# Performance work log

Measured on AMD Instinct MI355X. Metric: run time of the kernel, lower is better.

Reference implementation:

```python
import jax, jax.numpy as jnp
import numpy as np

N, IN_DIM, N_HEADS, HID, OUT = 4096, 512, 8, 64, 128


def setup_inputs() -> dict:
    key = jax.random.key(0)
    k0, k1, k2, k3 = jax.random.split(key, 4)
    x = jax.random.normal(k0, (N, IN_DIM), dtype=jnp.float32)
    adj = jax.random.randint(k1, (N, N), 0, 2).astype(jnp.int32)
    Wh = jax.random.normal(k2, (N_HEADS, IN_DIM, HID), dtype=jnp.float32) * 0.02
    bh = jnp.zeros((N_HEADS, HID), dtype=jnp.float32)
    Wo = jax.random.normal(k3, (N_HEADS * HID, OUT), dtype=jnp.float32) * 0.02
    bo = jnp.zeros((OUT,), dtype=jnp.float32)
    return {"x": x, "adj": adj, "Wh": Wh, "bh": bh, "Wo": Wo, "bo": bo}


def _masked_attn(q, k, v, mask):
    # adjacency-masked scaled dot-product attention; q,k,v: [..., n, d]
    d = q.shape[-1]
    scores = jnp.einsum('...nd,...md->...nm', q, k) / jnp.sqrt(jnp.asarray(d, q.dtype))
    scores = jnp.where(mask, scores, jnp.asarray(-1e9, q.dtype))
    attn = jax.nn.softmax(scores, axis=-1)
    return jnp.einsum('...nm,...md->...nd', attn, v)


def reference(x, adj, Wh, bh, Wo, bo):
    mask = adj > 0  # [N, N]
    # per-head: Linear -> masked attention -> ELU (dropout is identity in eval)
    h = jnp.einsum('ni,hid->hnd', x, Wh) + bh[:, None, :]        # [H, N, D]
    heads = jax.nn.elu(_masked_attn(h, h, h, mask[None]))        # [H, N, D]
    cat = jnp.transpose(heads, (1, 0, 2)).reshape(x.shape[0], -1)  # [N, H*D]
    z = cat @ Wo + bo                                            # [N, OUT]
    out = jax.nn.elu(_masked_attn(z, z, z, mask))                # [N, OUT]
    return jax.nn.log_softmax(out, axis=1)
```

## Files before the change

### kernel.cpp

```cpp
#include <hip/hip_runtime.h>
#include <stdint.h>


#define NN 4096
#define IND 512
#define NH 8
#define HD 64
#define OD 128
#define S1 2
#define KSPLIT 8

typedef __bf16 bf16;
typedef bf16 bf16x8 __attribute__((ext_vector_type(8)));
typedef float f32x4 __attribute__((ext_vector_type(4)));
typedef unsigned short u16;
typedef unsigned long long u64;

__device__ __forceinline__ u16 f2bf(float f) {
  union { float f; unsigned u; } v; v.f = f;
  return (u16)((v.u + 0x7fffu + ((v.u >> 16) & 1u)) >> 16);
}

__device__ __forceinline__ f32x4 mfma16(bf16x8 a, bf16x8 b, f32x4 c) {
  return __builtin_amdgcn_mfma_f32_16x16x32_bf16(a, b, c, 0, 0, 0);
}

__global__ void k_h(const float* __restrict__ x, const float* __restrict__ Wh,
                    const float* __restrict__ bh, u16* __restrict__ h,
                    u16* __restrict__ hT) {
  const int head = blockIdx.y;
  const int d = threadIdx.x & 63;
  const int wv = threadIdx.x >> 6;
  const int n0 = blockIdx.x * 32 + wv * 8;
  const float* __restrict__ W = Wh + head * IND * HD;
  const float b0 = bh[head * HD + d];
  float acc[8];
  #pragma unroll
  for (int r = 0; r < 8; ++r) acc[r] = b0;
  #pragma unroll 2
  for (int i = 0; i < IND; i += 2) {
    const float w0 = W[(i + 0) * HD + d];
    const float w1 = W[(i + 1) * HD + d];
    #pragma unroll
    for (int r = 0; r < 8; ++r) {
      const float2 xv = *(const float2*)&x[(n0 + r) * IND + i];
      acc[r] += xv.x * w0 + xv.y * w1;
    }
  }
  #pragma unroll
  for (int r = 0; r < 8; ++r) {
    const u16 b = f2bf(acc[r]);
    h[(head * NN + n0 + r) * HD + d] = b;
    hT[(head * HD + d) * NN + n0 + r] = b;
  }
}

__global__ void k_mask(const int* __restrict__ adj, u64* __restrict__ mk) {
  const int row = blockIdx.x;
  const int wv = threadIdx.x >> 6;
  const int lane = threadIdx.x & 63;
  #pragma unroll
  for (int t = 0; t < 16; ++t) {
    const int w = wv * 16 + t;
    const u64 b = __ballot(adj[row * NN + w * 64 + lane] > 0);
    if (lane == 0) mk[row * 64 + w] = b;
  }
}

__global__ void k_wot(const float* __restrict__ Wo, u16* __restrict__ WoT) {
  const int t = blockIdx.x * 256 + threadIdx.x;
  const int k = t >> 7, o = t & 127;
  WoT[o * IND + k] = f2bf(Wo[t]);
}

__launch_bounds__(64)
__global__ void k_attn1s(const u16* __restrict__ h, const u16* __restrict__ hT,
                         const u64* __restrict__ mk, float* __restrict__ Opart,
                         float* __restrict__ lpart) {
  const int head = blockIdx.y;
  const int sp = blockIdx.z;
  const int lane = threadIdx.x & 63;
  const int q0 = blockIdx.x * 16;
  const int lj = lane & 15;
  const int lg = lane >> 4;
  __shared__ u16 Pl[16][40];
  u16* __restrict__ Pw = &Pl[0][0];

  const u16* __restrict__ hh = h + head * NN * HD;
  const u16* __restrict__ ht = hT + head * HD * NN;

  bf16x8 qf[2];
  #pragma unroll
  for (int c = 0; c < 2; ++c)
    qf[c] = *(const bf16x8*)&hh[(q0 + lj) * HD + c * 32 + lg * 8];

  float lsum[4] = {0.f, 0.f, 0.f, 0.f};
  f32x4 O[4];
  #pragma unroll
  for (int dt = 0; dt < 4; ++dt) O[dt] = f32x4{0.f, 0.f, 0.f, 0.f};

  const int kt0 = sp * (NN / 32 / S1);
  for (int kt = kt0; kt < kt0 + NN / 32 / S1; ++kt) {
    const int kv0 = kt * 32;
    bf16x8 kf0[2], kf1[2];
    #pragma unroll
    for (int c = 0; c < 2; ++c) {
      kf0[c] = *(const bf16x8*)&hh[(kv0 + lj) * HD + c * 32 + lg * 8];
      kf1[c] = *(const bf16x8*)&hh[(kv0 + 16 + lj) * HD + c * 32 + lg * 8];
    }
    f32x4 s0 = f32x4{0.f, 0.f, 0.f, 0.f}, s1 = f32x4{0.f, 0.f, 0.f, 0.f};
    s0 = mfma16(qf[0], kf0[0], s0);
    s0 = mfma16(qf[1], kf0[1], s0);
    s1 = mfma16(qf[0], kf1[0], s1);
    s1 = mfma16(qf[1], kf1[1], s1);

    const int wi = kv0 >> 6;
    const int bsh = kv0 & 63;
    #pragma unroll
    for (int r = 0; r < 4; ++r) {
      const int qrow = q0 + lg * 4 + r;
      const u64 w = mk[qrow * 64 + wi];
      const float p0 = ((w >> (bsh + lj)) & 1ull) ? __expf(s0[r] * 0.125f) : 0.f;
      const float p1 = ((w >> (bsh + 16 + lj)) & 1ull) ? __expf(s1[r] * 0.125f) : 0.f;
      lsum[r] += p0 + p1;
      Pw[(lg * 4 + r) * 40 + lj] = f2bf(p0);
      Pw[(lg * 4 + r) * 40 + 16 + lj] = f2bf(p1);
    }
    asm volatile("s_waitcnt lgkmcnt(0)" ::: "memory");
    const bf16x8 pf = *(const bf16x8*)&Pw[lj * 40 + lg * 8];
    #pragma unroll
    for (int dt = 0; dt < 4; ++dt) {
      const bf16x8 vf = *(const bf16x8*)&ht[(dt * 16 + lj) * NN + kv0 + lg * 8];
      O[dt] = mfma16(pf, vf, O[dt]);
    }
    asm volatile("s_waitcnt lgkmcnt(0)" ::: "memory");
  }

  #pragma unroll
  for (int r = 0; r < 4; ++r) {
    float ls = lsum[r];
    ls += __shfl_xor(ls, 1);
    ls += __shfl_xor(ls, 2);
    ls += __shfl_xor(ls, 4);
    ls += __shfl_xor(ls, 8);
    const int row = q0 + lg * 4 + r;
    if (lj == 0) lpart[(sp * NH + head) * NN + row] = ls;
    #pragma unroll
    for (int dt = 0; dt < 4; ++dt)
      Opart[((size_t)(sp * NH + head) * NN + row) * HD + dt * 16 + lj] = O[dt][r];
  }
}

__launch_bounds__(64)
__global__ void k_ared1(const float* __restrict__ Opart,
                        const float* __restrict__ lpart, u16* __restrict__ cat) {
  const int row = blockIdx.x;
  const int head = blockIdx.y;
  const int lane = threadIdx.x & 63;
  float o = 0.f, ls = 0.f;
  #pragma unroll
  for (int s = 0; s < S1; ++s) {
    o += Opart[((size_t)(s * NH + head) * NN + row) * HD + lane];
    ls += lpart[(s * NH + head) * NN + row];
  }
  float v = o / ls;
  v = v > 0.f ? v : expm1f(v);
  cat[row * (NH * HD) + head * HD + lane] = f2bf(v);
}

__launch_bounds__(64)
__global__ void k_zgemm(const u16* __restrict__ cat, const u16* __restrict__ WoT,
                        const float* __restrict__ bo, u16* __restrict__ z,
                        u16* __restrict__ zT) {
  const int lane = threadIdx.x & 63;
  const int r0 = blockIdx.x * 16;
  const int lj = lane & 15, lg = lane >> 4;
  f32x4 acc[8];
  #pragma unroll
  for (int nt = 0; nt < 8; ++nt) acc[nt] = f32x4{0.f, 0.f, 0.f, 0.f};
  for (int kc = 0; kc < 16; ++kc) {
    const bf16x8 a = *(const bf16x8*)&cat[(r0 + lj) * IND + kc * 32 + lg * 8];
    #pragma unroll
    for (int nt = 0; nt < 8; ++nt) {
      const bf16x8 b = *(const bf16x8*)&WoT[(nt * 16 + lj) * IND + kc * 32 + lg * 8];
      acc[nt] = mfma16(a, b, acc[nt]);
    }
  }
  #pragma unroll
  for (int nt = 0; nt < 8; ++nt) {
    #pragma unroll
    for (int r = 0; r < 4; ++r) {
      const int row = r0 + lg * 4 + r;
      const int col = nt * 16 + lj;
      const u16 bv = f2bf(acc[nt][r] + bo[col]);
      z[row * OD + col] = bv;
      zT[col * NN + row] = bv;
    }
  }
}

__launch_bounds__(64)
__global__ void k_attn2s(const u16* __restrict__ z, const u16* __restrict__ zT,
                         const u64* __restrict__ mk, float* __restrict__ Opart,
                         float* __restrict__ lpart) {
  const int lane = threadIdx.x & 63;
  const int q0 = blockIdx.x * 16;
  const int sp = blockIdx.y;
  const int lj = lane & 15, lg = lane >> 4;
  __shared__ u16 Pl[16][40];
  u16* __restrict__ Pw = &Pl[0][0];

  bf16x8 qf[4];
  #pragma unroll
  for (int c = 0; c < 4; ++c)
    qf[c] = *(const bf16x8*)&z[(q0 + lj) * OD + c * 32 + lg * 8];

  float lsum[4] = {0.f, 0.f, 0.f, 0.f};
  f32x4 O[8];
  #pragma unroll
  for (int dt = 0; dt < 8; ++dt) O[dt] = f32x4{0.f, 0.f, 0.f, 0.f};

  const float scl = 0.08838834764831845f;
  const int kt0 = sp * (NN / 32 / KSPLIT);
  for (int kt = kt0; kt < kt0 + NN / 32 / KSPLIT; ++kt) {
    const int kv0 = kt * 32;
    f32x4 s0 = f32x4{0.f, 0.f, 0.f, 0.f}, s1 = f32x4{0.f, 0.f, 0.f, 0.f};
    #pragma unroll
    for (int c = 0; c < 4; ++c) {
      const bf16x8 k0 = *(const bf16x8*)&z[(kv0 + lj) * OD + c * 32 + lg * 8];
      s0 = mfma16(qf[c], k0, s0);
    }
    #pragma unroll
    for (int c = 0; c < 4; ++c) {
      const bf16x8 k1 = *(const bf16x8*)&z[(kv0 + 16 + lj) * OD + c * 32 + lg * 8];
      s1 = mfma16(qf[c], k1, s1);
    }

    const int wi = kv0 >> 6;
    const int bsh = kv0 & 63;
    #pragma unroll
    for (int r = 0; r < 4; ++r) {
      const int qrow = q0 + lg * 4 + r;
      const u64 w = mk[qrow * 64 + wi];
      const float p0 = ((w >> (bsh + lj)) & 1ull) ? __expf(s0[r] * scl) : 0.f;
      const float p1 = ((w >> (bsh + 16 + lj)) & 1ull) ? __expf(s1[r] * scl) : 0.f;
      lsum[r] += p0 + p1;
      Pw[(lg * 4 + r) * 40 + lj] = f2bf(p0);
      Pw[(lg * 4 + r) * 40 + 16 + lj] = f2bf(p1);
    }
    asm volatile("s_waitcnt lgkmcnt(0)" ::: "memory");
    const bf16x8 pf = *(const bf16x8*)&Pw[lj * 40 + lg * 8];
    #pragma unroll
    for (int dt = 0; dt < 8; ++dt) {
      const bf16x8 vf = *(const bf16x8*)&zT[(dt * 16 + lj) * NN + kv0 + lg * 8];
      O[dt] = mfma16(pf, vf, O[dt]);
    }
    asm volatile("s_waitcnt lgkmcnt(0)" ::: "memory");
  }

  #pragma unroll
  for (int r = 0; r < 4; ++r) {
    float ls = lsum[r];
    ls += __shfl_xor(ls, 1);
    ls += __shfl_xor(ls, 2);
    ls += __shfl_xor(ls, 4);
    ls += __shfl_xor(ls, 8);
    const int row = q0 + lg * 4 + r;
    if (lj == 0) lpart[sp * NN + row] = ls;
    #pragma unroll
    for (int dt = 0; dt < 8; ++dt)
      Opart[((size_t)sp * NN + row) * OD + dt * 16 + lj] = O[dt][r];
  }
}

__launch_bounds__(64)
__global__ void k_ared(const float* __restrict__ Opart,
                       const float* __restrict__ lpart, float* __restrict__ out) {
  const int row = blockIdx.x;
  const int lane = threadIdx.x & 63;
  float o0 = 0.f, o1 = 0.f, ls = 0.f;
  #pragma unroll
  for (int s = 0; s < KSPLIT; ++s) {
    o0 += Opart[((size_t)s * NN + row) * OD + lane];
    o1 += Opart[((size_t)s * NN + row) * OD + 64 + lane];
    ls += lpart[s * NN + row];
  }
  const float inv = 1.f / ls;
  float v0 = o0 * inv; v0 = v0 > 0.f ? v0 : expm1f(v0);
  float v1 = o1 * inv; v1 = v1 > 0.f ? v1 : expm1f(v1);
  float rmax = fmaxf(v0, v1);
  rmax = fmaxf(rmax, __shfl_xor(rmax, 1));
  rmax = fmaxf(rmax, __shfl_xor(rmax, 2));
  rmax = fmaxf(rmax, __shfl_xor(rmax, 4));
  rmax = fmaxf(rmax, __shfl_xor(rmax, 8));
  rmax = fmaxf(rmax, __shfl_xor(rmax, 16));
  rmax = fmaxf(rmax, __shfl_xor(rmax, 32));
  float se = __expf(v0 - rmax) + __expf(v1 - rmax);
  se += __shfl_xor(se, 1);
  se += __shfl_xor(se, 2);
  se += __shfl_xor(se, 4);
  se += __shfl_xor(se, 8);
  se += __shfl_xor(se, 16);
  se += __shfl_xor(se, 32);
  const float lse = rmax + logf(se);
  out[row * OD + lane] = v0 - lse;
  out[row * OD + 64 + lane] = v1 - lse;
}

extern "C" void kernel_launch(void* const* d_in, const int* in_sizes, int n_in,
                              void* d_out, int out_size, void* d_ws, size_t ws_size,
                              hipStream_t stream) {
  const float* x   = (const float*)d_in[0];
  const int*   adj = (const int*)d_in[1];
  const float* Wh  = (const float*)d_in[2];
  const float* bh  = (const float*)d_in[3];
  const float* Wo  = (const float*)d_in[4];
  const float* bo  = (const float*)d_in[5];
  float* out = (float*)d_out;

  char* ws = (char*)d_ws;
  u16*   h     = (u16*)(ws);
  u16*   hT    = (u16*)(ws + (4ull << 20));
  u64*   mk    = (u64*)(ws + (8ull << 20));
  u16*   cat   = (u16*)(ws + (10ull << 20));
  u16*   WoT   = (u16*)(ws + (14ull << 20));
  u16*   z     = (u16*)(ws + (15ull << 20));
  u16*   zT    = (u16*)(ws + (16ull << 20));
  float* Opart = (float*)(ws + (17ull << 20));
  float* lpart = (float*)(ws + (33ull << 20));

  k_mask<<<NN, 256, 0, stream>>>(adj, mk);
  k_wot<<<256, 256, 0, stream>>>(Wo, WoT);
  k_h<<<dim3(NN / 32, NH), 256, 0, stream>>>(x, Wh, bh, h, hT);
  k_attn1s<<<dim3(NN / 16, NH, S1), 64, 0, stream>>>(h, hT, mk, Opart, lpart);
  k_ared1<<<dim3(NN, NH), 64, 0, stream>>>(Opart, lpart, cat);
  k_zgemm<<<NN / 16, 64, 0, stream>>>(cat, WoT, bo, z, zT);
  k_attn2s<<<dim3(NN / 16, KSPLIT), 64, 0, stream>>>(z, zT, mk, Opart, lpart);
  k_ared<<<NN, 64, 0, stream>>>(Opart, lpart, out);
}
```

Baseline: 616.0 us.

## Prefetch V tiles, double-buffer P, store split partials in bf16, raise split counts

The attention kernels now load the V fragments at the start of each key tile, and they alternate between two LDS P buffers so the trailing wait can be dropped. The goal is to overlap global latency with the score computation. Partial outputs are stored as bf16 to halve the traffic of writing and reducing them. The split factors are doubled to launch more blocks, and the first reduction kernel now processes a whole row with 256 threads. The costs are extra register pressure, rounding error in the partial sums, and more partial data to reduce.

```diff
diff --git a/kernel.cpp b/kernel.cpp
--- a/kernel.cpp
+++ b/kernel.cpp
@@ -7,8 +7,8 @@
 #define NH 8
 #define HD 64
 #define OD 128
-#define S1 2
-#define KSPLIT 8
+#define S1 4
+#define KSPLIT 16
 
 typedef __bf16 bf16;
 typedef bf16 bf16x8 __attribute__((ext_vector_type(8)));
@@ -19,6 +19,9 @@
 __device__ __forceinline__ u16 f2bf(float f) {
   union { float f; unsigned u; } v; v.f = f;
   return (u16)((v.u + 0x7fffu + ((v.u >> 16) & 1u)) >> 16);
+}
+__device__ __forceinline__ float bf2f(u16 b) {
+  union { unsigned u; float f; } v; v.u = ((unsigned)b) << 16; return v.f;
 }
 
 __device__ __forceinline__ f32x4 mfma16(bf16x8 a, bf16x8 b, f32x4 c) {
@@ -75,7 +78,7 @@
 
 __launch_bounds__(64)
 __global__ void k_attn1s(const u16* __restrict__ h, const u16* __restrict__ hT,
-                         const u64* __restrict__ mk, float* __restrict__ Opart,
+                         const u64* __restrict__ mk, u16* __restrict__ Opart,
                          float* __restrict__ lpart) {
   const int head = blockIdx.y;
   const int sp = blockIdx.z;
@@ -83,8 +86,7 @@
   const int q0 = blockIdx.x * 16;
   const int lj = lane & 15;
   const int lg = lane >> 4;
-  __shared__ u16 Pl[16][40];
-  u16* __restrict__ Pw = &Pl[0][0];
+  __shared__ u16 Pl[2][16][40];
 
   const u16* __restrict__ hh = h + head * NN * HD;
   const u16* __restrict__ ht = hT + head * HD * NN;
@@ -99,15 +101,22 @@
   #pragma unroll
   for (int dt = 0; dt < 4; ++dt) O[dt] = f32x4{0.f, 0.f, 0.f, 0.f};
 
-  const int kt0 = sp * (NN / 32 / S1);
-  for (int kt = kt0; kt < kt0 + NN / 32 / S1; ++kt) {
+  const int ktn = NN / 32 / S1;
+  const int kt0 = sp * ktn;
+  for (int kt = kt0; kt < kt0 + ktn; ++kt) {
     const int kv0 = kt * 32;
+    u16* __restrict__ Pw = &Pl[kt & 1][0][0];
     bf16x8 kf0[2], kf1[2];
     #pragma unroll
     for (int c = 0; c < 2; ++c) {
       kf0[c] = *(const bf16x8*)&hh[(kv0 + lj) * HD + c * 32 + lg * 8];
       kf1[c] = *(const bf16x8*)&hh[(kv0 + 16 + lj) * HD + c * 32 + lg * 8];
     }
+    bf16x8 vf[4];
+    #pragma unroll
+    for (int dt = 0; dt < 4; ++dt)
+      vf[dt] = *(const bf16x8*)&ht[(dt * 16 + lj) * NN + kv0 + lg * 8];
+
     f32x4 s0 = f32x4{0.f, 0.f, 0.f, 0.f}, s1 = f32x4{0.f, 0.f, 0.f, 0.f};
     s0 = mfma16(qf[0], kf0[0], s0);
     s0 = mfma16(qf[1], kf0[1], s0);
@@ -129,11 +138,7 @@
     asm volatile("s_waitcnt lgkmcnt(0)" ::: "memory");
     const bf16x8 pf = *(const bf16x8*)&Pw[lj * 40 + lg * 8];
     #pragma unroll
-    for (int dt = 0; dt < 4; ++dt) {
-      const bf16x8 vf = *(const bf16x8*)&ht[(dt * 16 + lj) * NN + kv0 + lg * 8];
-      O[dt] = mfma16(pf, vf, O[dt]);
-    }
-    asm volatile("s_waitcnt lgkmcnt(0)" ::: "memory");
+    for (int dt = 0; dt < 4; ++dt) O[dt] = mfma16(pf, vf[dt], O[dt]);
   }
 
   #pragma unroll
@@ -147,25 +152,31 @@
     if (lj == 0) lpart[(sp * NH + head) * NN + row] = ls;
     #pragma unroll
     for (int dt = 0; dt < 4; ++dt)
-      Opart[((size_t)(sp * NH + head) * NN + row) * HD + dt * 16 + lj] = O[dt][r];
-  }
-}
-
-__launch_bounds__(64)
-__global__ void k_ared1(const float* __restrict__ Opart,
+      Opart[((size_t)(sp * NH + head) * NN + row) * HD + dt * 16 + lj] =
+          f2bf(O[dt][r]);
+  }
+}
+
+__launch_bounds__(256)
+__global__ void k_ared1(const u16* __restrict__ Opart,
                         const float* __restrict__ lpart, u16* __restrict__ cat) {
   const int row = blockIdx.x;
-  const int head = blockIdx.y;
-  const int lane = threadIdx.x & 63;
-  float o = 0.f, ls = 0.f;
-  #pragma unroll
-  for (int s = 0; s < S1; ++s) {
-    o += Opart[((size_t)(s * NH + head) * NN + row) * HD + lane];
-    ls += lpart[(s * NH + head) * NN + row];
-  }
-  float v = o / ls;
-  v = v > 0.f ? v : expm1f(v);
-  cat[row * (NH * HD) + head * HD + lane] = f2bf(v);
+  const int t = threadIdx.x;
+  #pragma unroll
+  for (int half = 0; half < 2; ++half) {
+    const int c = t + half * 256;
+    const int head = c >> 6;
+    const int cl = c & 63;
+    float o = 0.f, ls = 0.f;
+    #pragma unroll
+    for (int s = 0; s < S1; ++s) {
+      o += bf2f(Opart[((size_t)(s * NH + head) * NN + row) * HD + cl]);
+      ls += lpart[(s * NH + head) * NN + row];
+    }
+    float v = o / ls;
+    v = v > 0.f ? v : expm1f(v);
+    cat[row * (NH * HD) + c] = f2bf(v);
+  }
 }
 
 __launch_bounds__(64)
@@ -201,14 +212,13 @@
 
 __launch_bounds__(64)
 __global__ void k_attn2s(const u16* __restrict__ z, const u16* __restrict__ zT,
-                         const u64* __restrict__ mk, float* __restrict__ Opart,
+                         const u64* __restrict__ mk, u16* __restrict__ Opart,
                          float* __restrict__ lpart) {
   const int lane = threadIdx.x & 63;
   const int q0 = blockIdx.x * 16;
   const int sp = blockIdx.y;
   const int lj = lane & 15, lg = lane >> 4;
-  __shared__ u16 Pl[16][40];
-  u16* __restrict__ Pw = &Pl[0][0];
+  __shared__ u16 Pl[2][16][40];
 
   bf16x8 qf[4];
   #pragma unroll
@@ -221,9 +231,16 @@
   for (int dt = 0; dt < 8; ++dt) O[dt] = f32x4{0.f, 0.f, 0.f, 0.f};
 
   const float scl = 0.08838834764831845f;
-  const int kt0 = sp * (NN / 32 / KSPLIT);
-  for (int kt = kt0; kt < kt0 + NN / 32 / KSPLIT; ++kt) {
+  const int ktn = NN / 32 / KSPLIT;
+  const int kt0 = sp * ktn;
+  for (int kt = kt0; kt < kt0 + ktn; ++kt) {
     const int kv0 = kt * 32;
+    u16* __restrict__ Pw = &Pl[kt & 1][0][0];
+    bf16x8 vf[8];
+    #pragma unroll
+    for (int dt = 0; dt < 8; ++dt)
+      vf[dt] = *(const bf16x8*)&zT[(dt * 16 + lj) * NN + kv0 + lg * 8];
+
     f32x4 s0 = f32x4{0.f, 0.f, 0.f, 0.f}, s1 = f32x4{0.f, 0.f, 0.f, 0.f};
     #pragma unroll
     for (int c = 0; c < 4; ++c) {
@@ -251,11 +268,7 @@
     asm volatile("s_waitcnt lgkmcnt(0)" ::: "memory");
     const bf16x8 pf = *(const bf16x8*)&Pw[lj * 40 + lg * 8];
     #pragma unroll
-    for (int dt = 0; dt < 8; ++dt) {
-      const bf16x8 vf = *(const bf16x8*)&zT[(dt * 16 + lj) * NN + kv0 + lg * 8];
-      O[dt] = mfma16(pf, vf, O[dt]);
-    }
-    asm volatile("s_waitcnt lgkmcnt(0)" ::: "memory");
+    for (int dt = 0; dt < 8; ++dt) O[dt] = mfma16(pf, vf[dt], O[dt]);
   }
 
   #pragma unroll
@@ -269,20 +282,20 @@
     if (lj == 0) lpart[sp * NN + row] = ls;
     #pragma unroll
     for (int dt = 0; dt < 8; ++dt)
-      Opart[((size_t)sp * NN + row) * OD + dt * 16 + lj] = O[dt][r];
+      Opart[((size_t)sp * NN + row) * OD + dt * 16 + lj] = f2bf(O[dt][r]);
   }
 }
 
 __launch_bounds__(64)
-__global__ void k_ared(const float* __restrict__ Opart,
+__global__ void k_ared(const u16* __restrict__ Opart,
                        const float* __restrict__ lpart, float* __restrict__ out) {
   const int row = blockIdx.x;
   const int lane = threadIdx.x & 63;
   float o0 = 0.f, o1 = 0.f, ls = 0.f;
   #pragma unroll
   for (int s = 0; s < KSPLIT; ++s) {
-    o0 += Opart[((size_t)s * NN + row) * OD + lane];
-    o1 += Opart[((size_t)s * NN + row) * OD + 64 + lane];
+    o0 += bf2f(Opart[((size_t)s * NN + row) * OD + lane]);
+    o1 += bf2f(Opart[((size_t)s * NN + row) * OD + 64 + lane]);
     ls += lpart[s * NN + row];
   }
   const float inv = 1.f / ls;
@@ -326,14 +339,14 @@
   u16*   WoT   = (u16*)(ws + (14ull << 20));
   u16*   z     = (u16*)(ws + (15ull << 20));
   u16*   zT    = (u16*)(ws + (16ull << 20));
-  float* Opart = (float*)(ws + (17ull << 20));
+  u16*   Opart = (u16*)(ws + (17ull << 20));
   float* lpart = (float*)(ws + (33ull << 20));
 
   k_mask<<<NN, 256, 0, stream>>>(adj, mk);
   k_wot<<<256, 256, 0, stream>>>(Wo, WoT);
   k_h<<<dim3(NN / 32, NH), 256, 0, stream>>>(x, Wh, bh, h, hT);
   k_attn1s<<<dim3(NN / 16, NH, S1), 64, 0, stream>>>(h, hT, mk, Opart, lpart);
-  k_ared1<<<dim3(NN, NH), 64, 0, stream>>>(Opart, lpart, cat);
+  k_ared1<<<NN, 256, 0, stream>>>(Opart, lpart, cat);
   k_zgemm<<<NN / 16, 64, 0, stream>>>(cat, WoT, bo, z, zT);
   k_attn2s<<<dim3(NN / 16, KSPLIT), 64, 0, stream>>>(z, zT, mk, Opart, lpart);
   k_ared<<<NN, 64, 0, stream>>>(Opart, lpart, out);
```

After: 607.0 us. Within noise of the previous version (-1.5%).
